# Performance work log

Hardware: AMD Instinct MI355X
Metric: run time of the kernel (lower is better)

Reference implementation:

```python
import jax, jax.numpy as jnp
import numpy as np

RPE_LEN = 14  # rpe_length
HEADS = 10
HDIM = 64
EMBED = 640
DFF = 2560


def layer_norm(x, g, b, eps=1e-5):
    mu = jnp.mean(x, axis=-1, keepdims=True)
    var = jnp.var(x, axis=-1, keepdims=True)
    return (x - mu) * jax.lax.rsqrt(var + eps) * g + b


def rpe_embeddings(table_v, table_h, N):
    """RelativePosition2D.forward(N, N) -> [N, N, head_dim]."""
    L = N - 1
    s = int(L ** 0.5)  # 14 for N=197
    r = jnp.arange(L)
    dist_v = r[None, :] // s - r[:, None] // s
    dist_h = r[None, :] % s - r[:, None] % s
    idx_v = jnp.clip(dist_v, -RPE_LEN, RPE_LEN) + RPE_LEN + 1
    idx_h = jnp.clip(dist_h, -RPE_LEN, RPE_LEN) + RPE_LEN + 1
    # pad one row/col of zeros at the front (class token -> index 0)
    idx_v = jnp.pad(idx_v, ((1, 0), (1, 0)))
    idx_h = jnp.pad(idx_h, ((1, 0), (1, 0)))
    return table_v[idx_v] + table_h[idx_h]


def setup_inputs() -> dict:
    key = jax.random.key(0)
    ks = jax.random.split(key, 20)
    B, N, E, H, D, F = 64, 197, EMBED, HEADS, HDIM, DFF
    T = 2 * RPE_LEN + 2  # 30
    std = 0.02
    return {
        "x": jax.random.normal(ks[0], (B, N, E), jnp.float32),
        "ln1_g": jnp.ones((E,), jnp.float32),
        "ln1_b": jnp.zeros((E,), jnp.float32),
        "Wq": jax.random.normal(ks[1], (H * D, E), jnp.float32) * std,
        "Wk": jax.random.normal(ks[2], (H * D, E), jnp.float32) * std,
        "Wv": jax.random.normal(ks[3], (H * D, E), jnp.float32) * std,
        "Wp": jax.random.normal(ks[4], (E, H * D), jnp.float32) * std,
        "bp": jnp.zeros((E,), jnp.float32),
        "rpk_v": jax.random.normal(ks[5], (T, D), jnp.float32) * std,
        "rpk_h": jax.random.normal(ks[6], (T, D), jnp.float32) * std,
        "rpv_v": jax.random.normal(ks[7], (T, D), jnp.float32) * std,
        "rpv_h": jax.random.normal(ks[8], (T, D), jnp.float32) * std,
        "ln2_g": jnp.ones((E,), jnp.float32),
        "ln2_b": jnp.zeros((E,), jnp.float32),
        "W1": jax.random.normal(ks[9], (F, E), jnp.float32) * std,
        "b1": jnp.zeros((F,), jnp.float32),
        "W2": jax.random.normal(ks[10], (E, F), jnp.float32) * std,
        "b2": jnp.zeros((E,), jnp.float32),
    }


def reference(x, ln1_g, ln1_b, Wq, Wk, Wv, Wp, bp,
              rpk_v, rpk_h, rpv_v, rpv_h,
              ln2_g, ln2_b, W1, b1, W2, b2):
    B, N, E = x.shape
    H, D = HEADS, HDIM
    scale = D ** (-0.5)

    # --- attention block (pre-norm) ---
    residual = x
    h = layer_norm(x, ln1_g, ln1_b)
    q = (h @ Wq.T).reshape(B, N, H, D)
    k = (h @ Wk.T).reshape(B, N, H, D)
    v = (h @ Wv.T).reshape(B, N, H, D)

    attn = jnp.einsum('bnhd,bmhd->bhnm', q, k) * scale
    r_p_k = rpe_embeddings(rpk_v, rpk_h, N)          # [N, N, D]
    attn = attn + jnp.einsum('bnhd,nmd->bhnm', q, r_p_k) * scale
    attn = jax.nn.softmax(attn, axis=-1)

    o = jnp.einsum('bhnm,bmhd->bhnd', attn, v)
    r_p_v = rpe_embeddings(rpv_v, rpv_h, N)          # [N, N, D]
    o = o + jnp.einsum('bhnm,nmd->bhnd', attn, r_p_v)
    o = o.transpose(0, 2, 1, 3).reshape(B, N, H * D)
    x = residual + o @ Wp.T + bp

    # --- FFN block (pre-norm) ---
    residual = x
    h = layer_norm(x, ln2_g, ln2_b)
    h = jax.nn.gelu(h @ W1.T + b1, approximate=False)
    x = residual + h @ W2.T + b2
    return x
```

## Files before the change

kernel.cpp:

```cpp
#include <hip/hip_runtime.h>
#include <hip/hip_bf16.h>
#include <math.h>

#define NN   197
#define EE   640
#define HH   10
#define DD   64
#define FF   2560
#define MTOK (64 * 197)
#define RPE_T 30

typedef __hip_bfloat16 bf16;
typedef __attribute__((ext_vector_type(8))) __bf16 bf16x8;
typedef __attribute__((ext_vector_type(4))) float  floatx4;
typedef __attribute__((ext_vector_type(8))) unsigned short ushort8;

#define MFMA32(a, b, c) __builtin_amdgcn_mfma_f32_16x16x32_bf16(a, b, c, 0, 0, 0)

__device__ __forceinline__ float bfbits2f(unsigned short u) {
    union { unsigned int i; float f; } x; x.i = ((unsigned int)u) << 16; return x.f;
}
__device__ __forceinline__ unsigned short f2bf(float f) {
    bf16 t = __float2bfloat16(f);
    unsigned short u; __builtin_memcpy(&u, &t, 2); return u;
}
__device__ __forceinline__ void gld16(const bf16* g, bf16* l) {
    __builtin_amdgcn_global_load_lds(
        (const __attribute__((address_space(1))) unsigned int*)g,
        (__attribute__((address_space(3))) unsigned int*)l, 16, 0, 0);
}
__device__ __forceinline__ float gelu_f(float v) {
    float y = 0.7978845608f * (v + 0.044715f * v * v * v);
    float a = fabsf(y);
    float e = __expf(-2.f * a);
    float t = (1.f - e) / (1.f + e);
    t = (y < 0.f) ? -t : t;
    return 0.5f * v * (1.f + t);
}

__global__ void detect_kernel(const unsigned int* __restrict__ g, int* __restrict__ flag) {
    if (threadIdx.x == 0) flag[0] = (g[0] == 0x3F800000u) ? 1 : 0;
}

struct ConvDesc {
    const void* src[18];
    bf16*       dst[18];
    int         end8[18];
};

__global__ __launch_bounds__(256) void conv_fused(
    ConvDesc d, int total8, const int* __restrict__ flag)
{
    int c = blockIdx.x * 256 + threadIdx.x;
    if (c >= total8) return;
    int s = 0, start = 0;
#pragma unroll
    for (int i = 0; i < 17; ++i) {
        if (c >= d.end8[i]) { s = i + 1; start = d.end8[i]; }
    }
    int local = c - start;
    if (flag[0]) {
        const float* sp = (const float*)d.src[s] + (size_t)local * 8;
        bf16 t[8];
#pragma unroll
        for (int j = 0; j < 8; ++j) t[j] = __float2bfloat16(sp[j]);
        *(ushort8*)(d.dst[s] + (size_t)local * 8) = *(const ushort8*)t;
    } else {
        ((ushort8*)d.dst[s])[local] = ((const ushort8*)d.src[s])[local];
    }
}

__global__ __launch_bounds__(256) void rpetrans_kernel(
    const bf16* __restrict__ rvv, const bf16* __restrict__ rvh,
    unsigned short* __restrict__ rvvT, unsigned short* __restrict__ rvhT)
{
    int t = blockIdx.x * 256 + threadIdx.x;
    if (t < 64 * 32) {
        int d = t >> 5, tt = t & 31;
        rvvT[t] = (tt < RPE_T) ? ((const unsigned short*)rvv)[tt * 64 + d] : 0;
        rvhT[t] = (tt < RPE_T) ? ((const unsigned short*)rvh)[tt * 64 + d] : 0;
    }
}

__global__ __launch_bounds__(256) void selbuild_kernel(
    bf16* __restrict__ SelV, bf16* __restrict__ SelH)
{
    int t = blockIdx.x * 256 + threadIdx.x;
    if (t < 16 * 224) {
        int j = t / 224, m = t % 224;
        bool valid = (j < 14) && (m >= 1) && (m < 197);
        SelV[t] = __float2bfloat16((valid && (m - 1) / 14 == j) ? 1.f : 0.f);
        SelH[t] = __float2bfloat16((valid && (m - 1) % 14 == j) ? 1.f : 0.f);
    }
}

__global__ __launch_bounds__(256) void vtrans_kernel(
    const bf16* __restrict__ qkv, unsigned short* __restrict__ VtG)
{
    int bh = blockIdx.x;
    int b = bh / HH, h = bh % HH;
    unsigned short* dst = VtG + (size_t)bh * (64 * 224);
    for (int t = threadIdx.x; t < 224 * 8; t += 256) {
        int m = t >> 3, d8 = (t & 7) << 3;
        ushort8 val = {0, 0, 0, 0, 0, 0, 0, 0};
        if (m < NN)
            val = *(const ushort8*)(qkv + ((size_t)b * NN + m) * 1920 + 1280 + h * 64 + d8);
#pragma unroll
        for (int j = 0; j < 8; ++j) dst[(d8 + j) * 224 + m] = val[j];
    }
}

__global__ __launch_bounds__(256) void ln_kernel(
    const void* __restrict__ xb, size_t xrow0, int xdyn,
    const int* __restrict__ flag,
    const bf16* __restrict__ g, const bf16* __restrict__ b,
    bf16* __restrict__ out, int nrows)
{
    int row  = blockIdx.x * 4 + (threadIdx.x >> 6);
    if (row >= nrows) return;
    int lane = threadIdx.x & 63;
    const int f32 = xdyn && flag[0];
    const size_t base = (xrow0 + row) * (size_t)EE;
    float vals[10];
    float s = 0.f, ss = 0.f;
#pragma unroll
    for (int j = 0; j < 10; ++j) {
        int e = j * 64 + lane;
        float f = f32 ? ((const float*)xb)[base + e]
                      : (float)((const bf16*)xb)[base + e];
        vals[j] = f; s += f; ss += f * f;
    }
#pragma unroll
    for (int off = 32; off; off >>= 1) {
        s  += __shfl_xor(s, off);
        ss += __shfl_xor(ss, off);
    }
    float mean = s * (1.f / EE);
    float var  = ss * (1.f / EE) - mean * mean;
    float rs   = rsqrtf(var + 1e-5f);
#pragma unroll
    for (int j = 0; j < 10; ++j) {
        int e = j * 64 + lane;
        float hv = (vals[j] - mean) * rs * (float)g[e] + (float)b[e];
        out[(size_t)row * EE + e] = __float2bfloat16(hv);
    }
}

__global__ __launch_bounds__(256) void gemm128(
    const bf16* __restrict__ A, const bf16* __restrict__ B,
    const bf16* __restrict__ bias,
    const void* __restrict__ residb, size_t resid_row0, int resid_dyn,
    void* __restrict__ outb, size_t out_row0, int out_dyn,
    const int* __restrict__ flag,
    int M, int N, int K, int gelu)
{
    __shared__ bf16 At[2][128 * 32];
    __shared__ bf16 Bt[2][128 * 32];

    const int tid  = threadIdx.x;
    const int wave = tid >> 6, lane = tid & 63;
    const int quad = lane >> 4, l16 = lane & 15;
    const int wy = wave >> 1, wx = wave & 1;
    const int m0 = blockIdx.x * 128;
    const int n0 = blockIdx.y * 128;

    const int drow   = wave * 16 + (lane >> 2);
    const int gchunk = ((lane & 3) ^ ((lane >> 3) & 3)) * 8;
    const int ar0 = min(m0 + drow, M - 1);
    const int ar1 = min(m0 + 64 + drow, M - 1);
    const bf16* Ag0 = A + (size_t)ar0 * K + gchunk;
    const bf16* Ag1 = A + (size_t)ar1 * K + gchunk;
    const bf16* Bg0 = B + (size_t)(n0 + drow) * K + gchunk;
    const bf16* Bg1 = B + (size_t)(n0 + 64 + drow) * K + gchunk;
    bf16* At00 = &At[0][wave * 512];
    bf16* At01 = &At[0][2048 + wave * 512];
    bf16* At10 = &At[1][wave * 512];
    bf16* At11 = &At[1][2048 + wave * 512];
    bf16* Bt00 = &Bt[0][wave * 512];
    bf16* Bt01 = &Bt[0][2048 + wave * 512];
    bf16* Bt10 = &Bt[1][wave * 512];
    bf16* Bt11 = &Bt[1][2048 + wave * 512];

    const int swz = (quad ^ ((l16 >> 1) & 3)) * 8;

    floatx4 acc[4][4] = {};

    for (int k0 = 0; k0 < K; k0 += 64) {
        __syncthreads();
        gld16(Ag0 + k0,      At00);
        gld16(Ag1 + k0,      At01);
        gld16(Ag0 + k0 + 32, At10);
        gld16(Ag1 + k0 + 32, At11);
        gld16(Bg0 + k0,      Bt00);
        gld16(Bg1 + k0,      Bt01);
        gld16(Bg0 + k0 + 32, Bt10);
        gld16(Bg1 + k0 + 32, Bt11);
        __syncthreads();

#pragma unroll
        for (int kk = 0; kk < 2; ++kk) {
            bf16x8 af[4], bfr[4];
#pragma unroll
            for (int s = 0; s < 4; ++s)
                af[s] = *(const bf16x8*)(&At[kk][(wy * 64 + s * 16 + l16) * 32 + swz]);
#pragma unroll
            for (int t = 0; t < 4; ++t)
                bfr[t] = *(const bf16x8*)(&Bt[kk][(wx * 64 + t * 16 + l16) * 32 + swz]);
#pragma unroll
            for (int s = 0; s < 4; ++s)
#pragma unroll
                for (int t = 0; t < 4; ++t)
                    acc[s][t] = MFMA32(af[s], bfr[t], acc[s][t]);
        }
    }

    const int fr = resid_dyn && flag[0];
    const int fo = out_dyn && flag[0];
    float bv[4];
#pragma unroll
    for (int t = 0; t < 4; ++t)
        bv[t] = bias ? (float)bias[n0 + wx * 64 + t * 16 + l16] : 0.f;

#pragma unroll
    for (int s = 0; s < 4; ++s) {
#pragma unroll
        for (int i = 0; i < 4; ++i) {
            int m = m0 + wy * 64 + s * 16 + quad * 4 + i;
            if (m < M) {
                size_t rowoff_o = (out_row0 + m) * (size_t)N;
                size_t rowoff_r = (resid_row0 + m) * (size_t)N;
#pragma unroll
                for (int t = 0; t < 4; ++t) {
                    int n = n0 + wx * 64 + t * 16 + l16;
                    float v = acc[s][t][i] + bv[t];
                    if (gelu) v = gelu_f(v);
                    if (residb)
                        v += fr ? ((const float*)residb)[rowoff_r + n]
                                : (float)((const bf16*)residb)[rowoff_r + n];
                    if (fo) ((float*)outb)[rowoff_o + n] = v;
                    else    ((bf16*)outb)[rowoff_o + n]  = __float2bfloat16(v);
                }
            }
        }
    }
}

__global__ __launch_bounds__(256) void attn_kernel(
    const bf16* __restrict__ qkv,
    const bf16* __restrict__ tkv, const bf16* __restrict__ tkh,
    const unsigned short* __restrict__ rvvT,
    const unsigned short* __restrict__ rvhT,
    const unsigned short* __restrict__ VtG,
    const bf16* __restrict__ SelV, const bf16* __restrict__ SelH,
    bf16* __restrict__ o)
{
    __shared__ unsigned short Pm[64 * 232];
    __shared__ unsigned short PSv[64 * 40];
    __shared__ unsigned short PSh[64 * 40];
    __shared__ unsigned short QTv[64 * 32];
    __shared__ unsigned short QTh[64 * 32];

    const int tid  = threadIdx.x;
    const int wave = tid >> 6, lane = tid & 63;
    const int quad = lane >> 4, l16 = lane & 15;
    const int b  = blockIdx.x / HH, h = blockIdx.x % HH;
    const int qt = blockIdx.y;
    const size_t rowbase = (size_t)b * NN;

    for (int t = tid; t < 64 * 40; t += 256) { PSv[t] = 0; PSh[t] = 0; }
    for (int t = tid; t < 64 * 24; t += 256) Pm[(t / 24) * 232 + 208 + (t % 24)] = 0;
    __syncthreads();

    const int rA = qt * 64 + wave * 16 + l16;
    const bf16* qrow = qkv + (rowbase + min(rA, NN - 1)) * 1920 + h * 64;
    bf16x8 qa0 = *(const bf16x8*)(qrow + quad * 8);
    bf16x8 qa1 = *(const bf16x8*)(qrow + 32 + quad * 8);

    {
        floatx4 av[2] = {}, ah[2] = {};
#pragma unroll
        for (int ct = 0; ct < 2; ++ct) {
            int t = min(ct * 16 + l16, RPE_T - 1);
            av[ct] = MFMA32(qa0, *(const bf16x8*)(tkv + t * 64 + quad * 8), av[ct]);
            av[ct] = MFMA32(qa1, *(const bf16x8*)(tkv + t * 64 + 32 + quad * 8), av[ct]);
            ah[ct] = MFMA32(qa0, *(const bf16x8*)(tkh + t * 64 + quad * 8), ah[ct]);
            ah[ct] = MFMA32(qa1, *(const bf16x8*)(tkh + t * 64 + 32 + quad * 8), ah[ct]);
        }
#pragma unroll
        for (int ct = 0; ct < 2; ++ct)
#pragma unroll
            for (int i = 0; i < 4; ++i) {
                int row = wave * 16 + quad * 4 + i;
                QTv[row * 32 + ct * 16 + l16] = f2bf(av[ct][i]);
                QTh[row * 32 + ct * 16 + l16] = f2bf(ah[ct][i]);
            }
    }

    floatx4 sacc[13];
#pragma unroll
    for (int mt = 0; mt < 13; ++mt) {
        const bf16* krow = qkv + (rowbase + min(mt * 16 + l16, NN - 1)) * 1920
                           + 640 + h * 64;
        floatx4 a = {};
        a = MFMA32(qa0, *(const bf16x8*)(krow + quad * 8), a);
        a = MFMA32(qa1, *(const bf16x8*)(krow + 32 + quad * 8), a);
        sacc[mt] = a;
    }

    int nn4[4], jn4[4], in4[4];
#pragma unroll
    for (int i = 0; i < 4; ++i) {
        int n = qt * 64 + wave * 16 + quad * 4 + i;
        nn4[i] = n;
        jn4[i] = (n > 0) ? (n - 1) / 14 : 0;
        in4[i] = (n > 0) ? (n - 1) % 14 : 0;
    }
    float mx4[4] = {-3e38f, -3e38f, -3e38f, -3e38f};
#pragma unroll
    for (int mt = 0; mt < 13; ++mt) {
        int m = mt * 16 + l16;
        int jm = (m > 0) ? (m - 1) / 14 : 0;
        int im = (m > 0) ? (m - 1) % 14 : 0;
        bool mok = (m < NN);
#pragma unroll
        for (int i = 0; i < 4; ++i) {
            int row = wave * 16 + quad * 4 + i;
            int iv = (nn4[i] == 0 || m == 0) ? 0 : (jm - jn4[i] + 15);
            int ih = (nn4[i] == 0 || m == 0) ? 0 : (im - in4[i] + 15);
            float val = mok ? (sacc[mt][i] + bfbits2f(QTv[row * 32 + iv])
                               + bfbits2f(QTh[row * 32 + ih])) * 0.125f
                            : -3e38f;
            sacc[mt][i] = val;
            mx4[i] = fmaxf(mx4[i], val);
        }
    }
#pragma unroll
    for (int i = 0; i < 4; ++i)
#pragma unroll
        for (int off = 1; off < 16; off <<= 1)
            mx4[i] = fmaxf(mx4[i], __shfl_xor(mx4[i], off));

    float sm4[4] = {0.f, 0.f, 0.f, 0.f};
#pragma unroll
    for (int mt = 0; mt < 13; ++mt) {
#pragma unroll
        for (int i = 0; i < 4; ++i) {
            float p = __expf(sacc[mt][i] - mx4[i]);
            sm4[i] += p;
            Pm[(wave * 16 + quad * 4 + i) * 232 + mt * 16 + l16] = f2bf(p);
        }
    }
#pragma unroll
    for (int i = 0; i < 4; ++i)
#pragma unroll
        for (int off = 1; off < 16; off <<= 1)
            sm4[i] += __shfl_xor(sm4[i], off);

    floatx4 oacc[4] = {};
    floatx4 psv = {}, psh = {};
    const unsigned short* vt = VtG + (size_t)blockIdx.x * (64 * 224);
    for (int k0 = 0; k0 < 224; k0 += 32) {
        bf16x8 pa = *(const bf16x8*)(const void*)&Pm[(wave * 16 + l16) * 232 + k0 + quad * 8];
#pragma unroll
        for (int ct = 0; ct < 4; ++ct) {
            bf16x8 vb = *(const bf16x8*)(const void*)&vt[(ct * 16 + l16) * 224 + k0 + quad * 8];
            oacc[ct] = MFMA32(pa, vb, oacc[ct]);
        }
        psv = MFMA32(pa, *(const bf16x8*)(SelV + l16 * 224 + k0 + quad * 8), psv);
        psh = MFMA32(pa, *(const bf16x8*)(SelH + l16 * 224 + k0 + quad * 8), psh);
    }

#pragma unroll
    for (int i = 0; i < 4; ++i) {
        int row = wave * 16 + quad * 4 + i;
        int n = qt * 64 + row;
        if (n >= 1 && n < NN && l16 < 14) {
            int jn2 = (n - 1) / 14, in2 = (n - 1) % 14;
            PSv[row * 40 + (l16 - jn2 + 15)] = f2bf(psv[i]);
            PSh[row * 40 + (l16 - in2 + 15)] = f2bf(psh[i]);
        }
    }
    if (lane < 16) {
        int row = wave * 16 + lane;
        int n = qt * 64 + row;
        if (n < NN) {
            float p0 = (n == 0) ? sm4[0] : bfbits2f(Pm[row * 232]);
            PSv[row * 40] = f2bf(p0);
            PSh[row * 40] = f2bf(p0);
        }
    }

    {
        bf16x8 pav = *(const bf16x8*)(const void*)&PSv[(wave * 16 + l16) * 40 + quad * 8];
        bf16x8 pah = *(const bf16x8*)(const void*)&PSh[(wave * 16 + l16) * 40 + quad * 8];
#pragma unroll
        for (int ct = 0; ct < 4; ++ct) {
            bf16x8 bv  = *(const bf16x8*)(const void*)&rvvT[(ct * 16 + l16) * 32 + quad * 8];
            bf16x8 bh2 = *(const bf16x8*)(const void*)&rvhT[(ct * 16 + l16) * 32 + quad * 8];
            oacc[ct] = MFMA32(pav, bv,  oacc[ct]);
            oacc[ct] = MFMA32(pah, bh2, oacc[ct]);
        }
    }
#pragma unroll
    for (int i = 0; i < 4; ++i) {
        float rinv = 1.f / sm4[i];
        int row = wave * 16 + quad * 4 + i;
        int n = qt * 64 + row;
        if (n < NN) {
#pragma unroll
            for (int ct = 0; ct < 4; ++ct)
                o[(rowbase + n) * 640 + h * 64 + ct * 16 + l16] =
                    __float2bfloat16(oacc[ct][i] * rinv);
        }
    }
}

extern "C" void kernel_launch(void* const* d_in, const int* in_sizes, int n_in,
                              void* d_out, int out_size, void* d_ws, size_t ws_size,
                              hipStream_t stream)
{
    char* ws = (char*)d_ws;
    size_t off = 0;
    auto alloc = [&](size_t bytes) -> void* {
        void* p = ws + off;
        off += (bytes + 255) & ~(size_t)255;
        return p;
    };

    int* flag = (int*)alloc(256);
    bf16* xc   = (bf16*)alloc((size_t)MTOK * EE * 2);
    bf16* Wqc  = (bf16*)alloc((size_t)EE * EE * 2);
    bf16* Wkc  = (bf16*)alloc((size_t)EE * EE * 2);
    bf16* Wvc  = (bf16*)alloc((size_t)EE * EE * 2);
    bf16* Wpc  = (bf16*)alloc((size_t)EE * EE * 2);
    bf16* W1c  = (bf16*)alloc((size_t)FF * EE * 2);
    bf16* W2c  = (bf16*)alloc((size_t)EE * FF * 2);
    bf16* l1g  = (bf16*)alloc(EE * 2);
    bf16* l1b  = (bf16*)alloc(EE * 2);
    bf16* l2g  = (bf16*)alloc(EE * 2);
    bf16* l2b  = (bf16*)alloc(EE * 2);
    bf16* bpc  = (bf16*)alloc(EE * 2);
    bf16* b1c  = (bf16*)alloc(FF * 2);
    bf16* b2c  = (bf16*)alloc(EE * 2);
    bf16* rkv  = (bf16*)alloc(RPE_T * DD * 2);
    bf16* rkh  = (bf16*)alloc(RPE_T * DD * 2);
    bf16* rvv  = (bf16*)alloc(RPE_T * DD * 2);
    bf16* rvh  = (bf16*)alloc(RPE_T * DD * 2);
    unsigned short* rvvT = (unsigned short*)alloc(64 * 32 * 2);
    unsigned short* rvhT = (unsigned short*)alloc(64 * 32 * 2);
    bf16* SelV = (bf16*)alloc(16 * 224 * 2);
    bf16* SelH = (bf16*)alloc(16 * 224 * 2);
    const size_t cvt_end = off;

    int Bc = 0;
    const int cands[6] = {64, 32, 16, 8, 4, 2};
    for (int i = 0; i < 6; ++i) {
        size_t rows = (size_t)NN * cands[i];
        size_t need = cvt_end + rows * 10240 + (size_t)cands[i] * HH * 64 * 224 * 2 + 8192;
        if (need <= ws_size) { Bc = cands[i]; break; }
    }
    if (Bc == 0) return;

    const int nchunks = 64 / Bc;
    const int rows    = NN * Bc;
    bf16* h1   = (bf16*)alloc((size_t)rows * EE * 2);
    bf16* qkvb = (bf16*)alloc((size_t)rows * 1920 * 2);
    bf16* h3   = (bf16*)alloc((size_t)rows * FF * 2);
    unsigned short* VtG = (unsigned short*)alloc((size_t)Bc * HH * 64 * 224 * 2);

    detect_kernel<<<1, 64, 0, stream>>>((const unsigned int*)d_in[1], flag);
    {
        ConvDesc cd;
        const void* srcs[18] = { d_in[0], d_in[3], d_in[4], d_in[5], d_in[6],
                                 d_in[14], d_in[16], d_in[1], d_in[2], d_in[12],
                                 d_in[13], d_in[7], d_in[15], d_in[17], d_in[8],
                                 d_in[9], d_in[10], d_in[11] };
        bf16* dsts[18] = { xc, Wqc, Wkc, Wvc, Wpc, W1c, W2c, l1g, l1b, l2g,
                           l2b, bpc, b1c, b2c, rkv, rkh, rvv, rvh };
        int ns[18] = { MTOK * EE, EE * EE, EE * EE, EE * EE, EE * EE, FF * EE,
                       EE * FF, EE, EE, EE, EE, EE, FF, EE,
                       RPE_T * DD, RPE_T * DD, RPE_T * DD, RPE_T * DD };
        int cum = 0;
        for (int i = 0; i < 18; ++i) {
            cd.src[i] = srcs[i]; cd.dst[i] = dsts[i];
            cum += ns[i] / 8; cd.end8[i] = cum;
        }
        conv_fused<<<(cum + 255) / 256, 256, 0, stream>>>(cd, cum, flag);
    }
    rpetrans_kernel<<<8, 256, 0, stream>>>(rvv, rvh, rvvT, rvhT);
    selbuild_kernel<<<14, 256, 0, stream>>>(SelV, SelH);

    const int gM128 = (rows + 127) / 128;
    const int gLN   = (rows + 3) / 4;

    for (int c = 0; c < nchunks; ++c) {
        const size_t row0 = (size_t)c * rows;

        ln_kernel<<<gLN, 256, 0, stream>>>(xc, row0, 0, flag, l1g, l1b, h1, rows);

        gemm128<<<dim3(gM128, 1920 / 128), 256, 0, stream>>>(
            h1, Wqc, nullptr, nullptr, 0, 0, qkvb, 0, 0, flag, rows, 1920, EE, 0);

        vtrans_kernel<<<Bc * HH, 256, 0, stream>>>(qkvb, VtG);

        attn_kernel<<<dim3(Bc * HH, 4), 256, 0, stream>>>(
            qkvb, rkv, rkh, rvvT, rvhT, VtG, SelV, SelH, h1);

        gemm128<<<dim3(gM128, EE / 128), 256, 0, stream>>>(
            h1, Wpc, bpc, xc, row0, 0, d_out, row0, 1, flag, rows, EE, EE, 0);
    }

    for (int c = 0; c < nchunks; ++c) {
        const size_t row0 = (size_t)c * rows;

        ln_kernel<<<gLN, 256, 0, stream>>>(d_out, row0, 1, flag, l2g, l2b, h1, rows);

        gemm128<<<dim3(gM128, FF / 128), 256, 0, stream>>>(
            h1, W1c, b1c, nullptr, 0, 0, h3, 0, 0, flag, rows, FF, EE, 1);

        gemm128<<<dim3(gM128, EE / 128), 256, 0, stream>>>(
            h3, W2c, b2c, d_out, row0, 1, d_out, row0, 1, flag, rows, EE, FF, 0);
    }
}
```

Before: 507.9 us.

## Double-buffer GEMM LDS tiles and swap grid axes for N-major block order

The GEMM kernel now keeps two LDS stages and issues global-to-LDS loads for the next K tile while the current one is being multiplied, which removes one barrier per iteration and hides load latency. The grid is also transposed so that consecutive blocks share the same A row tile and walk along N, aiming for better L2 reuse of activations. LDS use doubles to 64 KB per block, which may lower occupancy. The single barrier at the top of the loop has to protect both the write-after-read and the read-after-write hazards, and it depends on gld16 completion semantics at that barrier.

```diff
diff --git a/kernel.cpp b/kernel.cpp
--- a/kernel.cpp
+++ b/kernel.cpp
@@ -154,15 +154,15 @@
     const int* __restrict__ flag,
     int M, int N, int K, int gelu)
 {
-    __shared__ bf16 At[2][128 * 32];
-    __shared__ bf16 Bt[2][128 * 32];
+    __shared__ bf16 At[2][2][128 * 32];
+    __shared__ bf16 Bt[2][2][128 * 32];
 
     const int tid  = threadIdx.x;
     const int wave = tid >> 6, lane = tid & 63;
     const int quad = lane >> 4, l16 = lane & 15;
     const int wy = wave >> 1, wx = wave & 1;
-    const int m0 = blockIdx.x * 128;
-    const int n0 = blockIdx.y * 128;
+    const int n0 = blockIdx.x * 128;
+    const int m0 = blockIdx.y * 128;
 
     const int drow   = wave * 16 + (lane >> 2);
     const int gchunk = ((lane & 3) ^ ((lane >> 3) & 3)) * 8;
@@ -172,40 +172,49 @@
     const bf16* Ag1 = A + (size_t)ar1 * K + gchunk;
     const bf16* Bg0 = B + (size_t)(n0 + drow) * K + gchunk;
     const bf16* Bg1 = B + (size_t)(n0 + 64 + drow) * K + gchunk;
-    bf16* At00 = &At[0][wave * 512];
-    bf16* At01 = &At[0][2048 + wave * 512];
-    bf16* At10 = &At[1][wave * 512];
-    bf16* At11 = &At[1][2048 + wave * 512];
-    bf16* Bt00 = &Bt[0][wave * 512];
-    bf16* Bt01 = &Bt[0][2048 + wave * 512];
-    bf16* Bt10 = &Bt[1][wave * 512];
-    bf16* Bt11 = &Bt[1][2048 + wave * 512];
+    const int lo0 = wave * 512;
+    const int lo1 = 2048 + wave * 512;
 
     const int swz = (quad ^ ((l16 >> 1) & 3)) * 8;
 
     floatx4 acc[4][4] = {};
-
-    for (int k0 = 0; k0 < K; k0 += 64) {
+    const int nk = K >> 6;
+
+    {
+        gld16(Ag0,      &At[0][0][lo0]);
+        gld16(Ag1,      &At[0][0][lo1]);
+        gld16(Ag0 + 32, &At[0][1][lo0]);
+        gld16(Ag1 + 32, &At[0][1][lo1]);
+        gld16(Bg0,      &Bt[0][0][lo0]);
+        gld16(Bg1,      &Bt[0][0][lo1]);
+        gld16(Bg0 + 32, &Bt[0][1][lo0]);
+        gld16(Bg1 + 32, &Bt[0][1][lo1]);
+    }
+
+    for (int k = 0; k < nk; ++k) {
         __syncthreads();
-        gld16(Ag0 + k0,      At00);
-        gld16(Ag1 + k0,      At01);
-        gld16(Ag0 + k0 + 32, At10);
-        gld16(Ag1 + k0 + 32, At11);
-        gld16(Bg0 + k0,      Bt00);
-        gld16(Bg1 + k0,      Bt01);
-        gld16(Bg0 + k0 + 32, Bt10);
-        gld16(Bg1 + k0 + 32, Bt11);
-        __syncthreads();
-
+        if (k + 1 < nk) {
+            const int pp = (k + 1) & 1;
+            const int k0 = (k + 1) << 6;
+            gld16(Ag0 + k0,      &At[pp][0][lo0]);
+            gld16(Ag1 + k0,      &At[pp][0][lo1]);
+            gld16(Ag0 + k0 + 32, &At[pp][1][lo0]);
+            gld16(Ag1 + k0 + 32, &At[pp][1][lo1]);
+            gld16(Bg0 + k0,      &Bt[pp][0][lo0]);
+            gld16(Bg1 + k0,      &Bt[pp][0][lo1]);
+            gld16(Bg0 + k0 + 32, &Bt[pp][1][lo0]);
+            gld16(Bg1 + k0 + 32, &Bt[pp][1][lo1]);
+        }
+        const int pc = k & 1;
 #pragma unroll
         for (int kk = 0; kk < 2; ++kk) {
             bf16x8 af[4], bfr[4];
 #pragma unroll
             for (int s = 0; s < 4; ++s)
-                af[s] = *(const bf16x8*)(&At[kk][(wy * 64 + s * 16 + l16) * 32 + swz]);
+                af[s] = *(const bf16x8*)(&At[pc][kk][(wy * 64 + s * 16 + l16) * 32 + swz]);
 #pragma unroll
             for (int t = 0; t < 4; ++t)
-                bfr[t] = *(const bf16x8*)(&Bt[kk][(wx * 64 + t * 16 + l16) * 32 + swz]);
+                bfr[t] = *(const bf16x8*)(&Bt[pc][kk][(wx * 64 + t * 16 + l16) * 32 + swz]);
 #pragma unroll
             for (int s = 0; s < 4; ++s)
 #pragma unroll
@@ -498,7 +507,7 @@
 
         ln_kernel<<<gLN, 256, 0, stream>>>(xc, row0, 0, flag, l1g, l1b, h1, rows);
 
-        gemm128<<<dim3(gM128, 1920 / 128), 256, 0, stream>>>(
+        gemm128<<<dim3(1920 / 128, gM128), 256, 0, stream>>>(
             h1, Wqc, nullptr, nullptr, 0, 0, qkvb, 0, 0, flag, rows, 1920, EE, 0);
 
         vtrans_kernel<<<Bc * HH, 256, 0, stream>>>(qkvb, VtG);
@@ -506,7 +515,7 @@
         attn_kernel<<<dim3(Bc * HH, 4), 256, 0, stream>>>(
             qkvb, rkv, rkh, rvvT, rvhT, VtG, SelV, SelH, h1);
 
-        gemm128<<<dim3(gM128, EE / 128), 256, 0, stream>>>(
+        gemm128<<<dim3(EE / 128, gM128), 256, 0, stream>>>(
             h1, Wpc, bpc, xc, row0, 0, d_out, row0, 1, flag, rows, EE, EE, 0);
     }
 
@@ -515,10 +524,10 @@
 
         ln_kernel<<<gLN, 256, 0, stream>>>(d_out, row0, 1, flag, l2g, l2b, h1, rows);
 
-        gemm128<<<dim3(gM128, FF / 128), 256, 0, stream>>>(
+        gemm128<<<dim3(FF / 128, gM128), 256, 0, stream>>>(
             h1, W1c, b1c, nullptr, 0, 0, h3, 0, 0, flag, rows, FF, EE, 1);
 
-        gemm128<<<dim3(gM128, EE / 128), 256, 0, stream>>>(
+        gemm128<<<dim3(EE / 128, gM128), 256, 0, stream>>>(
             h3, W2c, b2c, d_out, row0, 1, d_out, row0, 1, flag, rows, EE, FF, 0);
     }
 }
```

Result: no change. 513.2 us (+1.0%).
